# Performance work log

Hardware: AMD Instinct MI355X
Metric: run time of the kernel (lower is better)

The kernel has to match this reference:

```python
import jax, jax.numpy as jnp
import numpy as np

IN_FEATURES = 11008
OUT_FEATURES = 4096
TOPK = 5504            # in_features * topk_ratio (0.5)
RECALL_THRES = 0.9
N_CACHE = 64           # modeled steady-state cache size


def setup_inputs() -> dict:
    key = jax.random.key(0)
    k1, k2, k3, k4 = jax.random.split(key, 4)
    x = jax.random.normal(k1, (1, 1, IN_FEATURES), dtype=jnp.float32)
    weight = jax.random.normal(k2, (OUT_FEATURES, IN_FEATURES), dtype=jnp.float32) * 0.02
    bias = jax.random.normal(k3, (OUT_FEATURES,), dtype=jnp.float32) * 0.02
    cached_indices = jax.random.randint(k4, (N_CACHE, TOPK), 0, IN_FEATURES, dtype=jnp.int64)
    return {"x": x, "weight": weight, "bias": bias, "cached_indices": cached_indices}


def reference(x, weight, bias, cached_indices):
    # decode path: bsz == seq == 1
    xf = x.reshape(-1, IN_FEATURES)                       # [1, in]
    x_mean = jnp.abs(xf).mean(axis=0)                     # [in]
    # top-k neuron selection (argsort descending -> top_k)
    _, topk_idx = jax.lax.top_k(x_mean, TOPK)             # [topk]
    topk_mask = jnp.zeros((IN_FEATURES,), dtype=bool).at[topk_idx].set(True)
    # rebuild cached boolean masks from cached index sets
    cached_masks = (
        jnp.zeros((N_CACHE, IN_FEATURES), dtype=bool)
        .at[jnp.arange(N_CACHE)[:, None], cached_indices]
        .set(True)
    )
    # recall of each cached mask against current top-k mask
    intersection = jnp.sum(cached_masks & topk_mask[None, :], axis=1)  # [n_cache]
    recalls = intersection.astype(jnp.float32) / TOPK
    best_idx = jnp.argmax(recalls)
    best_recall = recalls[best_idx]
    # cache hit -> reuse cached indices; miss -> use fresh top-k indices
    idx = jnp.where(best_recall >= RECALL_THRES, cached_indices[best_idx], topk_idx)
    # gather sparse column slice, then small GEMM + bias
    w_slice = weight[:, idx]                               # [out, topk]
    out = xf[:, idx] @ w_slice.T + bias                    # [1, out]
    return out.reshape(1, 1, OUT_FEATURES)
```

## Files before the change

kernel.cpp:

```cpp
#include <hip/hip_runtime.h>
#include <stdint.h>

#define IN_F   11008
#define OUT_F  4096
#define TOPK_K 5504
#define NCACHE 64
#define MASK_WORDS 344
#define NCHUNK 11


__device__ __forceinline__ unsigned absbits(float v) {
    return __float_as_uint(v) & 0x7fffffffu;
}

__global__ __launch_bounds__(1024) void k_select(const float* __restrict__ x,
                                                 unsigned* __restrict__ maskbits_g,
                                                 unsigned* __restrict__ score_g,
                                                 int* __restrict__ counts_g) {
    __shared__ unsigned hist[16][256];
    __shared__ unsigned csum[256];
    __shared__ unsigned sh_T, sh_rem, sh_totEq;
    __shared__ unsigned waveEq[NCHUNK][16];
    __shared__ unsigned waveEqPre[NCHUNK][16];

    const int tid  = threadIdx.x;
    const int wv   = tid >> 6;
    const int lane = tid & 63;
    const int nk   = (tid < IN_F - 10 * 1024) ? NCHUNK : NCHUNK - 1;

    unsigned key[NCHUNK];
#pragma unroll
    for (int c = 0; c < NCHUNK; ++c) {
        key[c] = 0u;
        if (c < nk) key[c] = absbits(x[c * 1024 + tid]);
    }

    for (int i = tid; i < IN_F; i += 1024) counts_g[i] = 0;
    if (tid == 0) *score_g = 0;

    unsigned prefix = 0, maskHi = 0, remaining = TOPK_K;

    for (int pass = 3; pass >= 0; --pass) {
        const int sh = pass * 8;
        for (int b = tid; b < 16 * 256; b += 1024) ((unsigned*)hist)[b] = 0;
        __syncthreads();
#pragma unroll
        for (int c = 0; c < NCHUNK; ++c) {
            if (c < nk && (key[c] & maskHi) == prefix)
                atomicAdd(&hist[wv][(key[c] >> sh) & 255], 1u);
        }
        __syncthreads();
        if (tid < 256) {
            unsigned s = 0;
#pragma unroll
            for (int w = 0; w < 16; ++w) s += hist[w][tid];
            csum[tid] = s;
        }
        __syncthreads();
        if (wv == 0) {
            unsigned c0 = csum[4 * lane + 0], c1 = csum[4 * lane + 1];
            unsigned c2 = csum[4 * lane + 2], c3 = csum[4 * lane + 3];
            unsigned S = c0 + c1 + c2 + c3;
#pragma unroll
            for (int off = 1; off < 64; off <<= 1) {
                unsigned v = __shfl_down(S, off, 64);
                if (lane + off < 64) S += v;
            }
            unsigned Sn = __shfl_down(S, 1, 64);
            if (lane == 63) Sn = 0;
            unsigned t3 = Sn + c3;
            unsigned t2 = t3 + c2;
            unsigned t1 = t2 + c1;
            unsigned t0 = t1 + c0;
            unsigned rem = remaining;
            if (t3 >= rem && Sn < rem) { sh_T = prefix | ((unsigned)(4 * lane + 3) << sh); sh_rem = rem - Sn; }
            if (t2 >= rem && t3 < rem) { sh_T = prefix | ((unsigned)(4 * lane + 2) << sh); sh_rem = rem - t3; }
            if (t1 >= rem && t2 < rem) { sh_T = prefix | ((unsigned)(4 * lane + 1) << sh); sh_rem = rem - t2; }
            if (t0 >= rem && t1 < rem) { sh_T = prefix | ((unsigned)(4 * lane + 0) << sh); sh_rem = rem - t1; }
        }
        __syncthreads();
        prefix = sh_T;
        maskHi |= 0xffu << sh;
        remaining = sh_rem;
    }

    const unsigned T = prefix;
    const unsigned eqTake = remaining;

    unsigned gtm = 0, eqm = 0;
#pragma unroll
    for (int c = 0; c < NCHUNK; ++c) {
        if (c < nk) {
            if (key[c] > T)       gtm |= 1u << c;
            else if (key[c] == T) eqm |= 1u << c;
        }
    }
#pragma unroll
    for (int c = 0; c < NCHUNK; ++c) {
        unsigned long long bal = __ballot((eqm >> c) & 1u);
        if (lane == 0) waveEq[c][wv] = (unsigned)__popcll(bal);
    }
    __syncthreads();
    if (tid < 64) {
        unsigned s = 0;
        for (int p = lane; p < NCHUNK * 16; p += 64) s += waveEq[p >> 4][p & 15];
#pragma unroll
        for (int off = 32; off > 0; off >>= 1) s += __shfl_down(s, off, 64);
        if (lane == 0) sh_totEq = s;
    }
    __syncthreads();
    const bool fast = (sh_totEq == eqTake);
    if (!fast) {
        if (tid == 0) {
            unsigned run = 0;
            for (int c = 0; c < NCHUNK; ++c)
                for (int w = 0; w < 16; ++w) { waveEqPre[c][w] = run; run += waveEq[c][w]; }
        }
        __syncthreads();
    }
#pragma unroll
    for (int c = 0; c < NCHUNK; ++c) {
        bool eq = (eqm >> c) & 1u;
        bool take;
        if (fast) {
            take = (((gtm >> c) & 1u) != 0u) || eq;
        } else {
            unsigned long long balEq = __ballot(eq);
            unsigned rank = waveEqPre[c][wv] + (unsigned)__popcll(balEq & ((1ull << lane) - 1ull));
            take = (((gtm >> c) & 1u) != 0u) || (eq && rank < eqTake);
        }
        unsigned long long balT = __ballot(take);
        int w0 = c * 32 + wv * 2;
        if (w0 < MASK_WORDS && lane == 0) {
            maskbits_g[w0]     = (unsigned)balT;
            maskbits_g[w0 + 1] = (unsigned)(balT >> 32);
        }
    }
}

__global__ __launch_bounds__(256) void k_recall(const int* __restrict__ cached,
                                                const unsigned* __restrict__ maskbits_g,
                                                unsigned* __restrict__ score_g) {
    __shared__ unsigned rowbits[MASK_WORDS];
    __shared__ unsigned wsum[4];
    const int r = blockIdx.x;
    const int tid = threadIdx.x;
    for (int w = tid; w < MASK_WORDS; w += 256) rowbits[w] = 0;
    __syncthreads();
    const int4* ci4 = (const int4*)(cached + (size_t)r * TOPK_K);
    for (int t = tid; t < TOPK_K / 4; t += 256) {
        int4 v = ci4[t];
        atomicOr(&rowbits[v.x >> 5], 1u << (v.x & 31));
        atomicOr(&rowbits[v.y >> 5], 1u << (v.y & 31));
        atomicOr(&rowbits[v.z >> 5], 1u << (v.z & 31));
        atomicOr(&rowbits[v.w >> 5], 1u << (v.w & 31));
    }
    __syncthreads();
    unsigned cnt = 0;
    for (int w = tid; w < MASK_WORDS; w += 256) cnt += __popc(rowbits[w] & maskbits_g[w]);
    for (int off = 32; off > 0; off >>= 1) cnt += __shfl_down(cnt, off, 64);
    if ((tid & 63) == 0) wsum[tid >> 6] = cnt;
    __syncthreads();
    if (tid == 0) {
        unsigned tot = wsum[0] + wsum[1] + wsum[2] + wsum[3];
        atomicMax(score_g, (tot << 6) | (unsigned)(63 - r));
    }
}

__global__ __launch_bounds__(256) void k_counts(const int* __restrict__ cached,
                                                const unsigned* __restrict__ score_g,
                                                int* __restrict__ counts_g) {
    unsigned score = *score_g;
    int best = 63 - (int)(score & 63u);
    int t = blockIdx.x * 256 + threadIdx.x;
    if (t < TOPK_K) atomicAdd(&counts_g[cached[best * TOPK_K + t]], 1);
}

#define ROWS_PER_BLOCK 8
__global__ __launch_bounds__(256) void k_gemv(const float* __restrict__ x,
                                              const float* __restrict__ W,
                                              const float* __restrict__ bias,
                                              const unsigned* __restrict__ maskbits_g,
                                              const unsigned* __restrict__ score_g,
                                              const int* __restrict__ counts_g,
                                              float* __restrict__ out) {
    __shared__ __align__(16) float xs[IN_F];
    const int tid = threadIdx.x;

    unsigned score = *score_g;
    unsigned inter = score >> 6;
    bool useCache = ((float)inter / (float)TOPK_K) >= 0.9f;

    const float4* x4 = (const float4*)x;
    for (int j = tid; j < IN_F / 4; j += 256) {
        float4 xv = x4[j];
        int base = j * 4;
        float c0, c1, c2, c3;
        if (useCache) {
            c0 = (float)counts_g[base + 0];
            c1 = (float)counts_g[base + 1];
            c2 = (float)counts_g[base + 2];
            c3 = (float)counts_g[base + 3];
        } else {
            unsigned wbits = maskbits_g[base >> 5];
            int sh = base & 31;
            c0 = (float)((wbits >> (sh + 0)) & 1u);
            c1 = (float)((wbits >> (sh + 1)) & 1u);
            c2 = (float)((wbits >> (sh + 2)) & 1u);
            c3 = (float)((wbits >> (sh + 3)) & 1u);
        }
        xs[base + 0] = xv.x * c0;
        xs[base + 1] = xv.y * c1;
        xs[base + 2] = xv.z * c2;
        xs[base + 3] = xv.w * c3;
    }
    __syncthreads();

    const int wv   = tid >> 6;
    const int lane = tid & 63;
    const int row0 = blockIdx.x * ROWS_PER_BLOCK + wv * 2;
    const int row1 = row0 + 1;
    const float4* w0p = (const float4*)(W + (size_t)row0 * IN_F);
    const float4* w1p = (const float4*)(W + (size_t)row1 * IN_F);
    const float4* xs4 = (const float4*)xs;

    float acc0 = 0.f, acc1 = 0.f;
#pragma unroll 4
    for (int j = lane; j < IN_F / 4; j += 64) {
        float4 xv = xs4[j];
        float4 a  = w0p[j];
        float4 b  = w1p[j];
        acc0 += xv.x * a.x + xv.y * a.y + xv.z * a.z + xv.w * a.w;
        acc1 += xv.x * b.x + xv.y * b.y + xv.z * b.z + xv.w * b.w;
    }
    for (int off = 32; off > 0; off >>= 1) {
        acc0 += __shfl_down(acc0, off, 64);
        acc1 += __shfl_down(acc1, off, 64);
    }
    if (lane == 0) {
        out[row0] = acc0 + bias[row0];
        out[row1] = acc1 + bias[row1];
    }
}

extern "C" void kernel_launch(void* const* d_in, const int* in_sizes, int n_in,
                              void* d_out, int out_size, void* d_ws, size_t ws_size,
                              hipStream_t stream) {
    const float* x      = (const float*)d_in[0];
    const float* W      = (const float*)d_in[1];
    const float* bias   = (const float*)d_in[2];
    const int*   cached = (const int*)d_in[3];
    float* out = (float*)d_out;

    char* ws = (char*)d_ws;
    unsigned* maskbits = (unsigned*)(ws + 0);
    unsigned* score    = (unsigned*)(ws + 1408);
    int*      counts   = (int*)(ws + 1536);

    k_select<<<1, 1024, 0, stream>>>(x, maskbits, score, counts);
    k_recall<<<NCACHE, 256, 0, stream>>>(cached, maskbits, score);
    k_counts<<<(TOPK_K + 255) / 256, 256, 0, stream>>>(cached, score, counts);
    k_gemv<<<OUT_F / ROWS_PER_BLOCK, 256, 0, stream>>>(x, W, bias, maskbits, score, counts, out);
}
```

Baseline: 285.4 us.

## Fuse cached-index count scatter into GEMV prologue and double rows per block

Removes the separate k_counts kernel and the global counts buffer. Each GEMV block now builds its masked x vector in shared memory directly, by zeroing it and atomically adding x[idx] for each cached index. Duplicate indices therefore accumulate, which matches the old count-weighted behaviour. The GEMV block grows to 512 threads covering 16 rows, so the per-block scatter prologue runs over half as many blocks. This saves a kernel launch and a global atomic pass, but every block now repeats the shared-memory atomic scatter of 5504 indices.

After: 280.1 us. About the same (-1.9%).

```diff
diff --git a/kernel.cpp b/kernel.cpp
--- a/kernel.cpp
+++ b/kernel.cpp
@@ -15,8 +15,7 @@
 
 __global__ __launch_bounds__(1024) void k_select(const float* __restrict__ x,
                                                  unsigned* __restrict__ maskbits_g,
-                                                 unsigned* __restrict__ score_g,
-                                                 int* __restrict__ counts_g) {
+                                                 unsigned* __restrict__ score_g) {
     __shared__ unsigned hist[16][256];
     __shared__ unsigned csum[256];
     __shared__ unsigned sh_T, sh_rem, sh_totEq;
@@ -35,7 +34,6 @@
         if (c < nk) key[c] = absbits(x[c * 1024 + tid]);
     }
 
-    for (int i = tid; i < IN_F; i += 1024) counts_g[i] = 0;
     if (tid == 0) *score_g = 0;
 
     unsigned prefix = 0, maskHi = 0, remaining = TOPK_K;
@@ -167,23 +165,15 @@
     }
 }
 
-__global__ __launch_bounds__(256) void k_counts(const int* __restrict__ cached,
-                                                const unsigned* __restrict__ score_g,
-                                                int* __restrict__ counts_g) {
-    unsigned score = *score_g;
-    int best = 63 - (int)(score & 63u);
-    int t = blockIdx.x * 256 + threadIdx.x;
-    if (t < TOPK_K) atomicAdd(&counts_g[cached[best * TOPK_K + t]], 1);
-}
-
-#define ROWS_PER_BLOCK 8
-__global__ __launch_bounds__(256) void k_gemv(const float* __restrict__ x,
-                                              const float* __restrict__ W,
-                                              const float* __restrict__ bias,
-                                              const unsigned* __restrict__ maskbits_g,
-                                              const unsigned* __restrict__ score_g,
-                                              const int* __restrict__ counts_g,
-                                              float* __restrict__ out) {
+#define ROWS_PER_BLOCK 16
+#define GEMV_THREADS   512
+__global__ __launch_bounds__(GEMV_THREADS) void k_gemv(const float* __restrict__ x,
+                                                       const float* __restrict__ W,
+                                                       const float* __restrict__ bias,
+                                                       const unsigned* __restrict__ maskbits_g,
+                                                       const unsigned* __restrict__ score_g,
+                                                       const int* __restrict__ cached,
+                                                       float* __restrict__ out) {
     __shared__ __align__(16) float xs[IN_F];
     const int tid = threadIdx.x;
 
@@ -191,28 +181,27 @@
     unsigned inter = score >> 6;
     bool useCache = ((float)inter / (float)TOPK_K) >= 0.9f;
 
-    const float4* x4 = (const float4*)x;
-    for (int j = tid; j < IN_F / 4; j += 256) {
-        float4 xv = x4[j];
-        int base = j * 4;
-        float c0, c1, c2, c3;
-        if (useCache) {
-            c0 = (float)counts_g[base + 0];
-            c1 = (float)counts_g[base + 1];
-            c2 = (float)counts_g[base + 2];
-            c3 = (float)counts_g[base + 3];
-        } else {
+    if (useCache) {
+        int best = 63 - (int)(score & 63u);
+        for (int i = tid; i < IN_F; i += GEMV_THREADS) xs[i] = 0.f;
+        __syncthreads();
+        const int* ci = cached + (size_t)best * TOPK_K;
+        for (int t = tid; t < TOPK_K; t += GEMV_THREADS) {
+            int idx = ci[t];
+            atomicAdd(&xs[idx], x[idx]);
+        }
+    } else {
+        const float4* x4 = (const float4*)x;
+        for (int j = tid; j < IN_F / 4; j += GEMV_THREADS) {
+            float4 xv = x4[j];
+            int base = j * 4;
             unsigned wbits = maskbits_g[base >> 5];
             int sh = base & 31;
-            c0 = (float)((wbits >> (sh + 0)) & 1u);
-            c1 = (float)((wbits >> (sh + 1)) & 1u);
-            c2 = (float)((wbits >> (sh + 2)) & 1u);
-            c3 = (float)((wbits >> (sh + 3)) & 1u);
-        }
-        xs[base + 0] = xv.x * c0;
-        xs[base + 1] = xv.y * c1;
-        xs[base + 2] = xv.z * c2;
-        xs[base + 3] = xv.w * c3;
+            xs[base + 0] = xv.x * (float)((wbits >> (sh + 0)) & 1u);
+            xs[base + 1] = xv.y * (float)((wbits >> (sh + 1)) & 1u);
+            xs[base + 2] = xv.z * (float)((wbits >> (sh + 2)) & 1u);
+            xs[base + 3] = xv.w * (float)((wbits >> (sh + 3)) & 1u);
+        }
     }
     __syncthreads();
 
@@ -255,10 +244,8 @@
     char* ws = (char*)d_ws;
     unsigned* maskbits = (unsigned*)(ws + 0);
     unsigned* score    = (unsigned*)(ws + 1408);
-    int*      counts   = (int*)(ws + 1536);
-
-    k_select<<<1, 1024, 0, stream>>>(x, maskbits, score, counts);
+
+    k_select<<<1, 1024, 0, stream>>>(x, maskbits, score);
     k_recall<<<NCACHE, 256, 0, stream>>>(cached, maskbits, score);
-    k_counts<<<(TOPK_K + 255) / 256, 256, 0, stream>>>(cached, score, counts);
-    k_gemv<<<OUT_F / ROWS_PER_BLOCK, 256, 0, stream>>>(x, W, bias, maskbits, score, counts, out);
-}
+    k_gemv<<<OUT_F / ROWS_PER_BLOCK, GEMV_THREADS, 0, stream>>>(x, W, bias, maskbits, score, cached, out);
+}
```
